# Performance work log

Hardware: AMD Instinct MI355X
Metric: run time of the kernel (lower is better)

## Reference

```python
import jax, jax.numpy as jnp
import numpy as np

B, T, D_MODEL, N_HEADS = 4, 2048, 1024, 16
HEAD_DIM = D_MODEL // N_HEADS  # 64
ROPE_BASE = 10000.0


def setup_inputs() -> dict:
    key = jax.random.key(0)
    k1, k2, k3 = jax.random.split(key, 3)
    x = jax.random.normal(k1, (B, T, D_MODEL), dtype=jnp.float32)
    # nn.Linear(d, 3d, bias=False) and nn.Linear(d, d, bias=False), stored as (in, out)
    w_qkv = jax.random.normal(k2, (D_MODEL, 3 * D_MODEL), dtype=jnp.float32) / np.sqrt(D_MODEL)
    w_proj = jax.random.normal(k3, (D_MODEL, D_MODEL), dtype=jnp.float32) / np.sqrt(D_MODEL)
    # standard RoPE tables: (T, HEAD_DIM/2)
    inv_freq = 1.0 / (ROPE_BASE ** (np.arange(0, HEAD_DIM, 2, dtype=np.float32) / HEAD_DIM))
    ang = np.arange(T, dtype=np.float32)[:, None] * inv_freq[None, :]
    cos = jnp.asarray(np.cos(ang), dtype=jnp.float32)
    sin = jnp.asarray(np.sin(ang), dtype=jnp.float32)
    return {"x": x, "cos": cos, "sin": sin, "w_qkv": w_qkv, "w_proj": w_proj}


def _apply_rope(x, cos, sin):
    # x: (B, H, T, D); cos/sin: (T, D/2) broadcast over (B, H)
    x1 = x[..., 0::2]
    x2 = x[..., 1::2]
    r1 = x1 * cos - x2 * sin
    r2 = x2 * cos + x1 * sin
    # interleave back: out[..., 0::2]=r1, out[..., 1::2]=r2
    return jnp.stack([r1, r2], axis=-1).reshape(x.shape)


def reference(x, cos, sin, w_qkv, w_proj):
    b, t, _ = x.shape
    qkv = (x @ w_qkv).reshape(b, t, 3, N_HEADS, HEAD_DIM).transpose(2, 0, 3, 1, 4)
    q, k, v = qkv[0], qkv[1], qkv[2]  # each (B, H, T, D)
    q = _apply_rope(q, cos[:t], sin[:t])
    k = _apply_rope(k, cos[:t], sin[:t])
    scale = 1.0 / jnp.sqrt(jnp.asarray(HEAD_DIM, dtype=x.dtype))
    scores = jnp.einsum("bhqd,bhkd->bhqk", q, k) * scale
    causal = jnp.tril(jnp.ones((t, t), dtype=bool))
    scores = jnp.where(causal, scores, jnp.finfo(scores.dtype).min)
    attn = jax.nn.softmax(scores, axis=-1)
    out = jnp.einsum("bhqk,bhkd->bhqd", attn, v)
    out = out.transpose(0, 2, 1, 3).reshape(b, t, D_MODEL)
    return out @ w_proj
```

## Files before the change

### kernel.cpp

```cpp
#include <hip/hip_runtime.h>
#include <cstdint>
#include <cstddef>

typedef __attribute__((ext_vector_type(8))) short bf16x8;
typedef __attribute__((ext_vector_type(4))) float f32x4;
typedef __attribute__((ext_vector_type(16))) float f32x16;
typedef __attribute__((ext_vector_type(4))) unsigned int u32x4;

#define B_ 4
#define T_ 2048
#define DM 1024
#define NH 16
#define HD 64

static __device__ __forceinline__ unsigned short f2bf(float f) {
  union { float f; unsigned int u; } v; v.f = f;
  unsigned int r = v.u + 0x7FFFu + ((v.u >> 16) & 1u);
  return (unsigned short)(r >> 16);
}
static __device__ __forceinline__ float exp2_fast(float x) {
  float r;
  asm volatile("v_exp_f32 %0, %1" : "=v"(r) : "v"(x));
  return r;
}
static __device__ __forceinline__ unsigned int cvt_pk_bf16(float a, float b) {
  unsigned int r;
  asm("v_cvt_pk_bf16_f32 %0, %1, %2" : "=v"(r) : "v"(a), "v"(b));
  return r;
}

static __device__ __forceinline__ void gll16(const void* g, void* l) {
  __builtin_amdgcn_global_load_lds(
      (const __attribute__((address_space(1))) void*)g,
      (__attribute__((address_space(3))) void*)l, 16, 0, 0);
}

#define BARRIER() do { asm volatile("" ::: "memory"); __builtin_amdgcn_s_barrier(); asm volatile("" ::: "memory"); } while (0)
#define WAITV0() asm volatile("s_waitcnt vmcnt(0)" ::: "memory")

__global__ __launch_bounds__(256) void prep_kernel(
    const float* __restrict__ x, unsigned short* __restrict__ x16,
    const float* __restrict__ w_qkv, unsigned short* __restrict__ wqkvT,
    const float* __restrict__ w_proj, unsigned short* __restrict__ wprojT) {
  __shared__ unsigned short tile[32][33];
  const int bid = blockIdx.x;
  const int tid = threadIdx.x;
  if (bid < 2048) {
    const int n8 = (B_ * T_ * DM) / 8;
    for (int i = bid * 256 + tid; i < n8; i += 2048 * 256) {
      const float4* p = (const float4*)(x + (size_t)i * 8);
      float4 a = p[0], b = p[1];
      u32x4 o;
      o[0] = cvt_pk_bf16(a.x, a.y);
      o[1] = cvt_pk_bf16(a.z, a.w);
      o[2] = cvt_pk_bf16(b.x, b.y);
      o[3] = cvt_pk_bf16(b.z, b.w);
      *(u32x4*)(x16 + (size_t)i * 8) = o;
    }
    return;
  }
  const float* in;
  unsigned short* out;
  int R, C, bx, by;
  if (bid < 5120) {
    const int b2 = bid - 2048;
    in = w_qkv; out = wqkvT; R = 1024; C = 3072;
    bx = b2 % 96; by = b2 / 96;
  } else {
    const int b2 = bid - 5120;
    in = w_proj; out = wprojT; R = 1024; C = 1024;
    bx = b2 % 32; by = b2 / 32;
  }
  const int c0 = bx * 32, r0 = by * 32;
  const int tx = tid & 31, ty = tid >> 5;
#pragma unroll
  for (int j = 0; j < 32; j += 8) {
    float v = in[(size_t)(r0 + ty + j) * C + c0 + tx];
    tile[tx][ty + j] = f2bf(v);
  }
  __syncthreads();
#pragma unroll
  for (int j = 0; j < 32; j += 8) {
    out[(size_t)(c0 + ty + j) * R + r0 + tx] = tile[ty + j][tx];
  }
}

#define GEMM_MAIN(As, Bs, Agl, Bgl, acc)                                     \
  {                                                                          \
    const char* gA = (const char*)(Agl) +                                    \
                     (size_t)(m0 + (tid >> 3)) * 2048 +                      \
                     (((tid & 7) ^ ((tid >> 3) & 7)) << 4);                  \
    const char* gB = (const char*)(Bgl) +                                    \
                     (size_t)(n0 + (tid >> 3)) * 2048 +                      \
                     (((tid & 7) ^ ((tid >> 3) & 7)) << 4);                  \
    for (int k0 = 0; k0 < 2048; k0 += 128) {                                 \
      _Pragma("unroll") for (int i = 0; i < 4; i++) {                        \
        gll16(gA + (size_t)i * 65536 + k0, (char*)(As) + i * 4096 + w * 1024);\
        gll16(gB + (size_t)i * 65536 + k0, (char*)(Bs) + i * 4096 + w * 1024);\
      }                                                                      \
      WAITV0();                                                              \
      BARRIER();                                                             \
      _Pragma("unroll") for (int kk = 0; kk < 2; kk++) {                     \
        bf16x8 af[4], bfr[4];                                                \
        const int ko = (kk * 64 + lg * 16) ^ ((lr & 7) << 4);                \
        _Pragma("unroll") for (int mi = 0; mi < 4; mi++)                     \
            af[mi] = *(const bf16x8*)((const char*)(As) +                    \
                                      (wr * 64 + mi * 16 + lr) * 128 + ko);  \
        _Pragma("unroll") for (int ni = 0; ni < 4; ni++)                     \
            bfr[ni] = *(const bf16x8*)((const char*)(Bs) +                   \
                                       (wc * 64 + ni * 16 + lr) * 128 + ko); \
        _Pragma("unroll") for (int mi = 0; mi < 4; mi++)                     \
            _Pragma("unroll") for (int ni = 0; ni < 4; ni++)                 \
                acc[mi][ni] = __builtin_amdgcn_mfma_f32_16x16x32_bf16(       \
                    af[mi], bfr[ni], acc[mi][ni], 0, 0, 0);                  \
      }                                                                      \
      BARRIER();                                                             \
    }                                                                        \
  }

__global__ __launch_bounds__(256, 3) void gemm_qkv(
    const unsigned short* __restrict__ A, const unsigned short* __restrict__ Bt,
    const float* __restrict__ cosT, const float* __restrict__ sinT,
    unsigned short* __restrict__ Qo, unsigned short* __restrict__ Ko,
    unsigned short* __restrict__ VTo) {
  __shared__ __align__(16) unsigned short As[128 * 64];
  __shared__ __align__(16) unsigned short Bs[128 * 64];
  const int bid = blockIdx.x;
  const int xcd = bid & 7;
  const int cc = bid >> 3;
  const int m0 = (xcd * 8 + (cc & 7)) * 128;
  const int n0 = (cc >> 3) * 128;
  const int tid = threadIdx.x;
  const int w = tid >> 6, l = tid & 63;
  const int wr = w >> 1, wc = w & 1;
  const int lr = l & 15, lg = l >> 4;
  f32x4 acc[4][4];
#pragma unroll
  for (int i = 0; i < 4; i++)
#pragma unroll
    for (int j = 0; j < 4; j++) acc[i][j] = (f32x4)0.f;

  GEMM_MAIN(As, Bs, A, Bt, acc)

  {
    float4* cosL4 = (float4*)As;
    float4* sinL4 = (float4*)Bs;
    const float4* cg = (const float4*)(cosT + (size_t)(m0 & 2047) * 32);
    const float4* sg = (const float4*)(sinT + (size_t)(m0 & 2047) * 32);
#pragma unroll
    for (int i = 0; i < 4; i++) {
      const int c = tid + i * 256;
      const int rw = c >> 3, f4 = c & 7;
      const int slot = rw * 8 + (f4 ^ (((rw >> 2) & 3) << 1));
      cosL4[slot] = cg[c];
      sinL4[slot] = sg[c];
    }
  }
  BARRIER();
  const float* cosL = (const float*)As;
  const float* sinL = (const float*)Bs;

#pragma unroll
  for (int mi = 0; mi < 4; mi++) {
#pragma unroll
    for (int ni = 0; ni < 4; ni++) {
      const int col = n0 + wc * 64 + ni * 16 + lr;
      const int which = col >> 10;
      const int hd = col & 1023;
      const int h = hd >> 6, d = hd & 63;
      const int fi = d >> 1;
      const float sgn = (lr & 1) ? 1.0f : -1.0f;
      const float qsc = (which == 0) ? 0.18033688f : 1.0f;
      float vv[4];
#pragma unroll
      for (int r = 0; r < 4; r++) {
        const int row = m0 + wr * 64 + mi * 16 + lg * 4 + r;
        float v = acc[mi][ni][r];
        if (which < 2) {
          float p = __shfl_xor(v, 1, 64);
          const int fj = fi ^ (((row >> 2) & 3) << 3);
          const int lo = (row & 127) * 32 + fj;
          v = (v * cosL[lo] + sgn * p * sinL[lo]) * qsc;
        }
        vv[r] = v;
      }
      const unsigned int pk0 = cvt_pk_bf16(vv[0], vv[1]);
      const unsigned int pk1 = cvt_pk_bf16(vv[2], vv[3]);
#pragma unroll
      for (int r = 0; r < 4; r++) {
        const int row = m0 + wr * 64 + mi * 16 + lg * 4 + r;
        const int b = row >> 11, tt = row & 2047;
        const unsigned int pk = (r < 2) ? pk0 : pk1;
        const unsigned short bv =
            (unsigned short)((r & 1) ? (pk >> 16) : (pk & 0xFFFFu));
        size_t bh = (size_t)(b * NH + h);
        if (which == 0)
          Qo[(bh * T_ + tt) * HD + d] = bv;
        else if (which == 1)
          Ko[(bh * T_ + tt) * HD + d] = bv;
        else
          VTo[(bh * HD + d) * T_ + tt] = bv;
      }
    }
  }
}

__global__ __launch_bounds__(256, 3) void gemm_proj(
    const unsigned short* __restrict__ A, const unsigned short* __restrict__ Bt,
    float* __restrict__ C) {
  __shared__ __align__(16) unsigned short As[128 * 64];
  __shared__ __align__(16) unsigned short Bs[128 * 64];
  const int bid = blockIdx.x;
  const int xcd = bid & 7;
  const int cc = bid >> 3;
  const int m0 = (xcd * 8 + cc / 8) * 128;
  const int n0 = (cc % 8) * 128;
  const int tid = threadIdx.x;
  const int w = tid >> 6, l = tid & 63;
  const int wr = w >> 1, wc = w & 1;
  const int lr = l & 15, lg = l >> 4;
  f32x4 acc[4][4];
#pragma unroll
  for (int i = 0; i < 4; i++)
#pragma unroll
    for (int j = 0; j < 4; j++) acc[i][j] = (f32x4)0.f;

  GEMM_MAIN(As, Bs, A, Bt, acc)

#pragma unroll
  for (int mi = 0; mi < 4; mi++) {
#pragma unroll
    for (int ni = 0; ni < 4; ni++) {
      const int col = n0 + wc * 64 + ni * 16 + lr;
#pragma unroll
      for (int r = 0; r < 4; r++) {
        const int row = m0 + wr * 64 + mi * 16 + lg * 4 + r;
        C[(size_t)row * 1024 + col] = acc[mi][ni][r];
      }
    }
  }
}

__global__ __launch_bounds__(256, 4) void attn_kernel(
    const unsigned short* __restrict__ Q, const unsigned short* __restrict__ K,
    const unsigned short* __restrict__ VT, unsigned short* __restrict__ O) {
  __shared__ __align__(16) unsigned short Ks[3][4096];
  __shared__ __align__(16) unsigned short Vs[2][4096];

  const int blk = blockIdx.x;
  const int bh = (blk & 7) * 8 + ((blk >> 3) & 7);
  const int r4 = blk >> 8, g4 = (blk >> 6) & 3;
  const int qt = (r4 == 0) ? (15 - g4)
               : (r4 == 1) ? (8 + g4)
               : (r4 == 2) ? (7 - g4)
                           : g4;
  const int b = bh >> 4, h = bh & 15;
  const int tid = threadIdx.x;
  const int w = tid >> 6, l = tid & 63;
  const int q31 = l & 31, h5 = l >> 5;
  const int q0w = qt * 128 + w * 32;
  const int q_abs = q0w + q31;

  const unsigned short* Qb = Q + (size_t)bh * T_ * HD;
  const char* Kc = (const char*)(K + (size_t)bh * T_ * HD);
  const char* Vc = (const char*)(VT + (size_t)bh * HD * T_);

  const int c0 = (w * 2) * 64 + l;
  const int c1 = (w * 2 + 1) * 64 + l;
  const int r0 = c0 >> 3, r1 = c1 >> 3;
  const int sw0 = ((c0 & 7) * 16) ^ ((r0 & 7) << 4);
  const int sw1 = ((c1 & 7) * 16) ^ ((r1 & 7) << 4);
  const char* pK0 = Kc + r0 * 128 + sw0;
  const char* pK1 = Kc + r1 * 128 + sw1;
  const char* pV0 = Vc + (size_t)r0 * (T_ * 2) + sw0;
  const char* pV1 = Vc + (size_t)r1 * (T_ * 2) + sw1;

#define SK(buf, tile)                                                       \
  do {                                                                      \
    size_t kb = (size_t)(tile) * 8192;                                      \
    gll16(pK0 + kb, (char*)Ks[buf] + (w * 2) * 1024);                       \
    gll16(pK1 + kb, (char*)Ks[buf] + (w * 2 + 1) * 1024);                   \
  } while (0)
#define SV(buf, tile)                                                       \
  do {                                                                      \
    size_t vb = (size_t)(tile) * 128;                                       \
    gll16(pV0 + vb, (char*)Vs[buf] + (w * 2) * 1024);                       \
    gll16(pV1 + vb, (char*)Vs[buf] + (w * 2 + 1) * 1024);                   \
  } while (0)

  bf16x8 qf[4];
#pragma unroll
  for (int ks4 = 0; ks4 < 4; ks4++)
    qf[ks4] = *(const bf16x8*)(Qb + (size_t)q_abs * HD + ks4 * 16 + h5 * 8);

  f32x16 ot0 = (f32x16)0.f, ot1 = (f32x16)0.f;
  float m_reg = -1e30f, lrow = 0.f;

  const int nt = 2 * qt + 2;
  const int jmax = q0w >> 6;

  SK(0, 0);
  SV(0, 0);
  if (nt > 1) {
    SV(1, 1);
    SK(1, 1);
  }
  if (nt > 2) SK(2, 2);

  int kcur = 0;
  for (int j = 0; j < nt; j++) {
    const int vcur = j & 1;
    if (j <= nt - 3) {
      asm volatile("s_waitcnt vmcnt(6)" ::: "memory");
    } else if (j == nt - 2) {
      asm volatile("s_waitcnt vmcnt(4)" ::: "memory");
    } else {
      asm volatile("s_waitcnt vmcnt(0)" ::: "memory");
    }
    BARRIER();
    if (j <= jmax) {
      f32x16 st[2];
      st[0] = (f32x16)0.f;
      st[1] = (f32x16)0.f;
      __builtin_amdgcn_s_setprio(1);
#pragma unroll
      for (int sub = 0; sub < 2; sub++) {
        const int row = sub * 32 + q31;
        const int sw = (row & 7) << 4;
#pragma unroll
        for (int ks4 = 0; ks4 < 4; ks4++) {
          bf16x8 kf = *(const bf16x8*)((const char*)Ks[kcur] + row * 128 +
                                       ((ks4 * 32 + h5 * 16) ^ sw));
          st[sub] = __builtin_amdgcn_mfma_f32_32x32x16_bf16(kf, qf[ks4],
                                                            st[sub], 0, 0, 0);
        }
      }
      __builtin_amdgcn_s_setprio(0);
      if (j == jmax) {
        const int t0 = j * 64;
#pragma unroll
        for (int sub = 0; sub < 2; sub++)
#pragma unroll
          for (int r = 0; r < 16; r++) {
            int kv_abs = t0 + sub * 32 + (r & 3) + 8 * (r >> 2) + 4 * h5;
            if (kv_abs > q_abs) st[sub][r] = -1e30f;
          }
      }
      float pmax;
      {
        float q0m = -1e30f, q1m = -1e30f;
#pragma unroll
        for (int r = 0; r < 16; r += 4) {
          q0m = fmaxf(q0m, fmaxf(fmaxf(st[0][r], st[0][r + 1]),
                                 fmaxf(st[0][r + 2], st[0][r + 3])));
          q1m = fmaxf(q1m, fmaxf(fmaxf(st[1][r], st[1][r + 1]),
                                 fmaxf(st[1][r + 2], st[1][r + 3])));
        }
        pmax = fmaxf(q0m, q1m);
      }
      pmax = fmaxf(pmax, __shfl_xor(pmax, 32, 64));
      const int defer = __all(pmax - m_reg <= 8.0f);
      if (!defer) {
        float mnew = fmaxf(m_reg, pmax);
        float alpha = exp2_fast(m_reg - mnew);
        m_reg = mnew;
        lrow *= alpha;
#pragma unroll
        for (int r = 0; r < 16; r++) {
          ot0[r] *= alpha;
          ot1[r] *= alpha;
        }
      }
      float rsum = 0.f;
#pragma unroll
      for (int sub = 0; sub < 2; sub++)
#pragma unroll
        for (int r = 0; r < 16; r++) {
          float p = exp2_fast(st[sub][r] - m_reg);
          st[sub][r] = p;
          rsum += p;
        }
      rsum += __shfl_xor(rsum, 32, 64);
      lrow += rsum;
      unsigned int pk[2][8];
#pragma unroll
      for (int sub = 0; sub < 2; sub++)
#pragma unroll
        for (int g = 0; g < 4; g++) {
          pk[sub][2 * g] = cvt_pk_bf16(st[sub][4 * g + 0], st[sub][4 * g + 1]);
          pk[sub][2 * g + 1] =
              cvt_pk_bf16(st[sub][4 * g + 2], st[sub][4 * g + 3]);
        }
      bf16x8 pf[4];
#pragma unroll
      for (int sub = 0; sub < 2; sub++)
#pragma unroll
        for (int s = 0; s < 2; s++) {
          unsigned int a0 = pk[sub][4 * s + 0], a1 = pk[sub][4 * s + 1];
          unsigned int b0 = pk[sub][4 * s + 2], b1 = pk[sub][4 * s + 3];
          unsigned int send0 = h5 ? a0 : b0, send1 = h5 ? a1 : b1;
          unsigned int sh0 = (unsigned int)__shfl_xor((int)send0, 32, 64);
          unsigned int sh1 = (unsigned int)__shfl_xor((int)send1, 32, 64);
          unsigned int ow0 = h5 ? b0 : a0, ow1 = h5 ? b1 : a1;
          u32x4 fu;
          fu[0] = h5 ? sh0 : ow0;
          fu[1] = h5 ? sh1 : ow1;
          fu[2] = h5 ? ow0 : sh0;
          fu[3] = h5 ? ow1 : sh1;
          pf[sub * 2 + s] = *(bf16x8*)&fu;
        }
      __builtin_amdgcn_s_setprio(1);
#pragma unroll
      for (int ks = 0; ks < 4; ks++) {
        const int colb = ks * 32 + h5 * 16;
        {
          const int row = q31;
          bf16x8 vf = *(const bf16x8*)((const char*)Vs[vcur] + row * 128 +
                                       (colb ^ ((row & 7) << 4)));
          ot0 = __builtin_amdgcn_mfma_f32_32x32x16_bf16(vf, pf[ks], ot0, 0, 0, 0);
        }
        {
          const int row = 32 + q31;
          bf16x8 vf = *(const bf16x8*)((const char*)Vs[vcur] + row * 128 +
                                       (colb ^ ((row & 7) << 4)));
          ot1 = __builtin_amdgcn_mfma_f32_32x32x16_bf16(vf, pf[ks], ot1, 0, 0, 0);
        }
      }
      __builtin_amdgcn_s_setprio(0);
    }
    BARRIER();
    if (j + 2 < nt) SV((j + 2) & 1, j + 2);
    if (j + 3 < nt) SK(kcur, j + 3);
    kcur = (kcur == 2) ? 0 : kcur + 1;
  }

  const float rcpl = 1.0f / lrow;
  unsigned short* Orow = O + ((size_t)b * T_ + q_abs) * DM + h * HD;
#pragma unroll
  for (int rg = 0; rg < 4; rg++) {
    uint2 s0;
    s0.x = cvt_pk_bf16(ot0[4 * rg + 0] * rcpl, ot0[4 * rg + 1] * rcpl);
    s0.y = cvt_pk_bf16(ot0[4 * rg + 2] * rcpl, ot0[4 * rg + 3] * rcpl);
    *(uint2*)(Orow + 8 * rg + 4 * h5) = s0;
    uint2 s1;
    s1.x = cvt_pk_bf16(ot1[4 * rg + 0] * rcpl, ot1[4 * rg + 1] * rcpl);
    s1.y = cvt_pk_bf16(ot1[4 * rg + 2] * rcpl, ot1[4 * rg + 3] * rcpl);
    *(uint2*)(Orow + 32 + 8 * rg + 4 * h5) = s1;
  }
#undef SK
#undef SV
}

extern "C" void kernel_launch(void* const* d_in, const int* in_sizes, int n_in,
                              void* d_out, int out_size, void* d_ws,
                              size_t ws_size, hipStream_t stream) {
  const float* x = (const float*)d_in[0];
  const float* cosT = (const float*)d_in[1];
  const float* sinT = (const float*)d_in[2];
  const float* w_qkv = (const float*)d_in[3];
  const float* w_proj = (const float*)d_in[4];
  float* out = (float*)d_out;

  char* ws = (char*)d_ws;
  unsigned short* x16 = (unsigned short*)(ws);
  unsigned short* wqkvT = (unsigned short*)(ws + (16 << 20));
  unsigned short* wprojT = (unsigned short*)(ws + (22 << 20));
  unsigned short* Qb = (unsigned short*)(ws + (24 << 20));
  unsigned short* Kb = (unsigned short*)(ws + (40 << 20));
  unsigned short* VTb = (unsigned short*)(ws + (56 << 20));
  unsigned short* Ob = x16;

  prep_kernel<<<6144, 256, 0, stream>>>(x, x16, w_qkv, wqkvT, w_proj, wprojT);
  gemm_qkv<<<1536, 256, 0, stream>>>(x16, wqkvT, cosT, sinT, Qb, Kb, VTb);
  attn_kernel<<<1024, 256, 0, stream>>>(Qb, Kb, VTb, Ob);
  gemm_proj<<<512, 256, 0, stream>>>(Ob, wprojT, out);
}
```

Baseline: 171.4 us.

## Double-buffer GEMM LDS tiles and triple-buffer V in attention

The shared GEMM main loop now double-buffers the A/B LDS tiles, issuing global-to-LDS loads for the next K step before computing the current one, instead of loading, waiting and computing serially. In attention, V gets a third LDS buffer so K and V share the same three-stage ring and are prefetched three tiles ahead. The extra LDS per block lowers the occupancy hints (GEMMs from 3 to 2 blocks, attention from 4 to 3), trading resident waves for overlap of memory and MFMA work.

```diff
diff --git a/kernel.cpp b/kernel.cpp
--- a/kernel.cpp
+++ b/kernel.cpp
@@ -36,7 +36,6 @@
 }
 
 #define BARRIER() do { asm volatile("" ::: "memory"); __builtin_amdgcn_s_barrier(); asm volatile("" ::: "memory"); } while (0)
-#define WAITV0() asm volatile("s_waitcnt vmcnt(0)" ::: "memory")
 
 __global__ __launch_bounds__(256) void prep_kernel(
     const float* __restrict__ x, unsigned short* __restrict__ x16,
@@ -85,7 +84,7 @@
   }
 }
 
-#define GEMM_MAIN(As, Bs, Agl, Bgl, acc)                                     \
+#define GEMM_MAIN2(As, Bs, Agl, Bgl, acc)                                    \
   {                                                                          \
     const char* gA = (const char*)(Agl) +                                    \
                      (size_t)(m0 + (tid >> 3)) * 2048 +                      \
@@ -93,21 +92,34 @@
     const char* gB = (const char*)(Bgl) +                                    \
                      (size_t)(n0 + (tid >> 3)) * 2048 +                      \
                      (((tid & 7) ^ ((tid >> 3) & 7)) << 4);                  \
-    for (int k0 = 0; k0 < 2048; k0 += 128) {                                 \
-      _Pragma("unroll") for (int i = 0; i < 4; i++) {                        \
-        gll16(gA + (size_t)i * 65536 + k0, (char*)(As) + i * 4096 + w * 1024);\
-        gll16(gB + (size_t)i * 65536 + k0, (char*)(Bs) + i * 4096 + w * 1024);\
+    _Pragma("unroll") for (int i = 0; i < 4; i++) {                          \
+      gll16(gA + (size_t)i * 65536, (char*)(As) + i * 4096 + w * 1024);      \
+      gll16(gB + (size_t)i * 65536, (char*)(Bs) + i * 4096 + w * 1024);      \
+    }                                                                        \
+    for (int t = 0; t < 16; t++) {                                           \
+      const int cur = (t & 1) << 14;                                         \
+      if (t < 15) {                                                          \
+        const int nxt = ((t + 1) & 1) << 14;                                 \
+        const int k0 = (t + 1) * 128;                                        \
+        _Pragma("unroll") for (int i = 0; i < 4; i++) {                      \
+          gll16(gA + (size_t)i * 65536 + k0,                                 \
+                (char*)(As) + nxt + i * 4096 + w * 1024);                    \
+          gll16(gB + (size_t)i * 65536 + k0,                                 \
+                (char*)(Bs) + nxt + i * 4096 + w * 1024);                    \
+        }                                                                    \
+        asm volatile("s_waitcnt vmcnt(8)" ::: "memory");                     \
+      } else {                                                               \
+        asm volatile("s_waitcnt vmcnt(0)" ::: "memory");                     \
       }                                                                      \
-      WAITV0();                                                              \
       BARRIER();                                                             \
       _Pragma("unroll") for (int kk = 0; kk < 2; kk++) {                     \
         bf16x8 af[4], bfr[4];                                                \
         const int ko = (kk * 64 + lg * 16) ^ ((lr & 7) << 4);                \
         _Pragma("unroll") for (int mi = 0; mi < 4; mi++)                     \
-            af[mi] = *(const bf16x8*)((const char*)(As) +                    \
+            af[mi] = *(const bf16x8*)((const char*)(As) + cur +              \
                                       (wr * 64 + mi * 16 + lr) * 128 + ko);  \
         _Pragma("unroll") for (int ni = 0; ni < 4; ni++)                     \
-            bfr[ni] = *(const bf16x8*)((const char*)(Bs) +                   \
+            bfr[ni] = *(const bf16x8*)((const char*)(Bs) + cur +             \
                                        (wc * 64 + ni * 16 + lr) * 128 + ko); \
         _Pragma("unroll") for (int mi = 0; mi < 4; mi++)                     \
             _Pragma("unroll") for (int ni = 0; ni < 4; ni++)                 \
@@ -118,13 +130,13 @@
     }                                                                        \
   }
 
-__global__ __launch_bounds__(256, 3) void gemm_qkv(
+__global__ __launch_bounds__(256, 2) void gemm_qkv(
     const unsigned short* __restrict__ A, const unsigned short* __restrict__ Bt,
     const float* __restrict__ cosT, const float* __restrict__ sinT,
     unsigned short* __restrict__ Qo, unsigned short* __restrict__ Ko,
     unsigned short* __restrict__ VTo) {
-  __shared__ __align__(16) unsigned short As[128 * 64];
-  __shared__ __align__(16) unsigned short Bs[128 * 64];
+  __shared__ __align__(16) unsigned short As[2 * 8192];
+  __shared__ __align__(16) unsigned short Bs[2 * 8192];
   const int bid = blockIdx.x;
   const int xcd = bid & 7;
   const int cc = bid >> 3;
@@ -140,7 +152,7 @@
 #pragma unroll
     for (int j = 0; j < 4; j++) acc[i][j] = (f32x4)0.f;
 
-  GEMM_MAIN(As, Bs, A, Bt, acc)
+  GEMM_MAIN2(As, Bs, A, Bt, acc)
 
   {
     float4* cosL4 = (float4*)As;
@@ -205,11 +217,11 @@
   }
 }
 
-__global__ __launch_bounds__(256, 3) void gemm_proj(
+__global__ __launch_bounds__(256, 2) void gemm_proj(
     const unsigned short* __restrict__ A, const unsigned short* __restrict__ Bt,
     float* __restrict__ C) {
-  __shared__ __align__(16) unsigned short As[128 * 64];
-  __shared__ __align__(16) unsigned short Bs[128 * 64];
+  __shared__ __align__(16) unsigned short As[2 * 8192];
+  __shared__ __align__(16) unsigned short Bs[2 * 8192];
   const int bid = blockIdx.x;
   const int xcd = bid & 7;
   const int cc = bid >> 3;
@@ -225,7 +237,7 @@
 #pragma unroll
     for (int j = 0; j < 4; j++) acc[i][j] = (f32x4)0.f;
 
-  GEMM_MAIN(As, Bs, A, Bt, acc)
+  GEMM_MAIN2(As, Bs, A, Bt, acc)
 
 #pragma unroll
   for (int mi = 0; mi < 4; mi++) {
@@ -241,11 +253,11 @@
   }
 }
 
-__global__ __launch_bounds__(256, 4) void attn_kernel(
+__global__ __launch_bounds__(256, 3) void attn_kernel(
     const unsigned short* __restrict__ Q, const unsigned short* __restrict__ K,
     const unsigned short* __restrict__ VT, unsigned short* __restrict__ O) {
   __shared__ __align__(16) unsigned short Ks[3][4096];
-  __shared__ __align__(16) unsigned short Vs[2][4096];
+  __shared__ __align__(16) unsigned short Vs[3][4096];
 
   const int blk = blockIdx.x;
   const int bh = (blk & 7) * 8 + ((blk >> 3) & 7);
@@ -302,16 +314,18 @@
   SK(0, 0);
   SV(0, 0);
   if (nt > 1) {
+    SK(1, 1);
     SV(1, 1);
-    SK(1, 1);
-  }
-  if (nt > 2) SK(2, 2);
-
-  int kcur = 0;
+  }
+  if (nt > 2) {
+    SK(2, 2);
+    SV(2, 2);
+  }
+
+  int cur3 = 0;
   for (int j = 0; j < nt; j++) {
-    const int vcur = j & 1;
     if (j <= nt - 3) {
-      asm volatile("s_waitcnt vmcnt(6)" ::: "memory");
+      asm volatile("s_waitcnt vmcnt(8)" ::: "memory");
     } else if (j == nt - 2) {
       asm volatile("s_waitcnt vmcnt(4)" ::: "memory");
     } else {
@@ -329,7 +343,7 @@
         const int sw = (row & 7) << 4;
 #pragma unroll
         for (int ks4 = 0; ks4 < 4; ks4++) {
-          bf16x8 kf = *(const bf16x8*)((const char*)Ks[kcur] + row * 128 +
+          bf16x8 kf = *(const bf16x8*)((const char*)Ks[cur3] + row * 128 +
                                        ((ks4 * 32 + h5 * 16) ^ sw));
           st[sub] = __builtin_amdgcn_mfma_f32_32x32x16_bf16(kf, qf[ks4],
                                                             st[sub], 0, 0, 0);
@@ -415,13 +429,13 @@
         const int colb = ks * 32 + h5 * 16;
         {
           const int row = q31;
-          bf16x8 vf = *(const bf16x8*)((const char*)Vs[vcur] + row * 128 +
+          bf16x8 vf = *(const bf16x8*)((const char*)Vs[cur3] + row * 128 +
                                        (colb ^ ((row & 7) << 4)));
           ot0 = __builtin_amdgcn_mfma_f32_32x32x16_bf16(vf, pf[ks], ot0, 0, 0, 0);
         }
         {
           const int row = 32 + q31;
-          bf16x8 vf = *(const bf16x8*)((const char*)Vs[vcur] + row * 128 +
+          bf16x8 vf = *(const bf16x8*)((const char*)Vs[cur3] + row * 128 +
                                        (colb ^ ((row & 7) << 4)));
           ot1 = __builtin_amdgcn_mfma_f32_32x32x16_bf16(vf, pf[ks], ot1, 0, 0, 0);
         }
@@ -429,9 +443,11 @@
       __builtin_amdgcn_s_setprio(0);
     }
     BARRIER();
-    if (j + 2 < nt) SV((j + 2) & 1, j + 2);
-    if (j + 3 < nt) SK(kcur, j + 3);
-    kcur = (kcur == 2) ? 0 : kcur + 1;
+    if (j + 3 < nt) {
+      SK(cur3, j + 3);
+      SV(cur3, j + 3);
+    }
+    cur3 = (cur3 == 2) ? 0 : cur3 + 1;
   }
 
   const float rcpl = 1.0f / lrow;
```

New measurement: 178.7 us. +4.3%, slower.
